# Kernel optimization log

Measured on AMD Instinct MI355X. Metric: run time of the kernel, lower is better.

## Reference

```python
import jax, jax.numpy as jnp
import numpy as np

B, C, H, W = 4, 16, 512, 512
OUT = 16
HID = 64
EPS = 1e-5


def _ln(x, g, b):
    mu = x.mean(-1, keepdims=True)
    v = x.var(-1, keepdims=True)
    return (x - mu) / jnp.sqrt(v + EPS) * g + b


def setup_inputs() -> dict:
    key = jax.random.key(0)
    ks = jax.random.split(key, 8)
    HW = H * W
    d = {}
    d['input'] = jax.random.normal(ks[0], (B, C, H, W), jnp.float32)
    d['W1'] = jax.random.normal(ks[1], (HID, HW), jnp.float32) * 0.01   # Linear1 weight [64, HW]
    d['b1'] = jnp.zeros((HID,), jnp.float32)
    d['ln1_g'] = jnp.ones((HID,), jnp.float32)
    d['ln1_b'] = jnp.zeros((HID,), jnp.float32)
    d['W2'] = jax.random.normal(ks[2], (HW, HID), jnp.float32) * 0.02   # Linear2 weight [HW, 64]
    d['b2'] = jnp.zeros((HW,), jnp.float32)
    d['ln2_g'] = jnp.ones((HW,), jnp.float32)
    d['ln2_b'] = jnp.zeros((HW,), jnp.float32)
    d['cw1'] = jax.random.normal(ks[3], (1, C, 1, 1), jnp.float32) * 0.1   # 1x1 conv C->1
    d['cb1'] = jnp.zeros((1,), jnp.float32)
    d['cw3'] = jax.random.normal(ks[4], (OUT, C, 3, 3), jnp.float32) * 0.05  # 3x3 conv C->OUT
    d['cb3'] = jnp.zeros((OUT,), jnp.float32)
    d['bn_g'] = jnp.ones((OUT,), jnp.float32)
    d['bn_b'] = jnp.zeros((OUT,), jnp.float32)
    return d


def reference(input, W1, b1, ln1_g, ln1_b, W2, b2, ln2_g, ln2_b, cw1, cb1, cw3, cb3, bn_g, bn_b):
    Bq, Cq, Hq, Wq = input.shape
    HW = Hq * Wq
    m = input.reshape(Bq, Cq, HW)
    # Linear1 -> LN -> ReLU  (per-channel over flattened spatial dim)
    h = jax.nn.relu(_ln(m @ W1.T + b1, ln1_g, ln1_b))            # [B, C, 64]
    # Linear2 -> LN -> ReLU
    m2 = jax.nn.relu(_ln(h @ W2.T + b2, ln2_g, ln2_b))           # [B, C, HW]
    m2 = m2.reshape(Bq, Cq, Hq, Wq)
    # 1x1 conv C -> 1
    score = jnp.einsum('bchw,oc->bohw', m2, cw1[:, :, 0, 0]) + cb1[:, None, None]  # [B,1,H,W]
    # keep_topk: ratio 0.25, no grad
    K = HW // 4
    flat = jax.lax.stop_gradient(score.reshape(Bq, HW))
    _, idx = jax.lax.top_k(flat, K)                               # [B, K]
    mask = jnp.zeros_like(flat).at[jnp.arange(Bq)[:, None], idx].set(1.0).reshape(Bq, 1, Hq, Wq)
    # boolean-mask gather: torch selects in ascending flat-index order
    idx_s = jnp.sort(idx, axis=1)                                 # [B, K]
    g = jnp.take_along_axis(m, idx_s[:, None, :], axis=2).reshape(Bq, Cq, Hq // 2, Wq // 2)
    # out_conv: 3x3 conv -> BatchNorm (batch stats, training mode) -> ReLU
    y = jax.lax.conv_general_dilated(g, cw3, (1, 1), [(1, 1), (1, 1)],
                                     dimension_numbers=('NCHW', 'OIHW', 'NCHW'))
    y = y + cb3[:, None, None]
    mu = y.mean((0, 2, 3), keepdims=True)
    v = y.var((0, 2, 3), keepdims=True)
    y = jax.nn.relu((y - mu) / jnp.sqrt(v + EPS) * bn_g[:, None, None] + bn_b[:, None, None])
    return (y, mask)
```

## Files before the change

### kernel.cpp

```cpp
#include <hip/hip_runtime.h>

#define HWN    262144
#define KSEL   65536
#define TIECAP 2048

#define OFF_H      0
#define OFF_DOT1   32768
#define OFF_G      65536
#define OFF_WBAR   98304
#define OFF_WB     98816
#define OFF_SB     99328
#define OFF_MU2    99360
#define OFF_ISIG2  99872
#define OFF_STATE  100384
#define OFF_HIST   100448
#define OFF_TIECNT 116832
#define OFF_CHCNT  116848
#define OFF_TIELST 116864
#define OFF_CHLST  149632
#define OFF_BCNT   182400
#define OFF_BOFF   186496
#define OFF_BNP    190592
#define OFF_BNC    452736
#define OFF_PART2  458752
#define OFF_HT     1015808
#define REGION2    1048576

#define PS_GRAM 4226
#define PS_DOT  4096

typedef double d4_t __attribute__((ext_vector_type(4)));
typedef float  f4v  __attribute__((ext_vector_type(4)));

__device__ __forceinline__ unsigned monokey(double s){
  unsigned long long b = (unsigned long long)__double_as_longlong(s);
  b = (b & 0x8000000000000000ULL) ? ~b : (b | 0x8000000000000000ULL);
  return (unsigned)(b >> 32);
}

__global__ void k_zero(unsigned* hist, unsigned* tiecnt, unsigned* chcnt, unsigned* state){
  int t = threadIdx.x;
  for (int i = t; i < 4096; i += 256) hist[i] = 0u;
  if (t < 4){
    tiecnt[t] = 0u; chcnt[t] = 0u;
    state[t*4+0] = 0u;
    state[t*4+1] = (unsigned)KSEL;
    state[t*4+2] = 0u;
    state[t*4+3] = 0u;
  }
}

__global__ __launch_bounds__(256) void k_mm(const float* __restrict__ W2,
                                            const float* __restrict__ b2,
                                            const float* __restrict__ inp,
                                            const float* __restrict__ W1,
                                            double* __restrict__ partG,
                                            double* __restrict__ partD,
                                            int pPerBlk, int NBH){
  int t = threadIdx.x;
  int w = t >> 6, l = t & 63;
  int q = l >> 4, m = l & 15;
  if ((int)blockIdx.x < NBH){
    int p0 = blockIdx.x * pPerBlk;
    d4_t acc0 = {0.,0.,0.,0.}, acc1 = {0.,0.,0.,0.}, acc2 = {0.,0.,0.,0.};
    d4_t acc3 = {0.,0.,0.,0.}, acc4 = {0.,0.,0.,0.}, acc44 = {0.,0.,0.,0.};
    const float* base = W2 + (size_t)(p0 + q)*64 + m;
    const float* b2p  = b2 + p0 + q;
    int wofs = w*16;
    int nCh = pPerBlk >> 2;
    for (int c = 0; c < nCh; c++){
      double f0 = (double)base[0];
      double f1 = (double)base[16];
      double f2 = (double)base[32];
      double f3 = (double)base[48];
      double fa = (double)base[wofs];
      double bb = (double)b2p[0];
      double f4 = (m == 0) ? bb : ((m == 1) ? 1.0 : 0.0);
      acc0 = __builtin_amdgcn_mfma_f64_16x16x4f64(fa, f0, acc0, 0, 0, 0);
      acc1 = __builtin_amdgcn_mfma_f64_16x16x4f64(fa, f1, acc1, 0, 0, 0);
      acc2 = __builtin_amdgcn_mfma_f64_16x16x4f64(fa, f2, acc2, 0, 0, 0);
      acc3 = __builtin_amdgcn_mfma_f64_16x16x4f64(fa, f3, acc3, 0, 0, 0);
      acc4 = __builtin_amdgcn_mfma_f64_16x16x4f64(fa, f4, acc4, 0, 0, 0);
      if (w == 0)
        acc44 = __builtin_amdgcn_mfma_f64_16x16x4f64(f4, f4, acc44, 0, 0, 0);
      base += 256; b2p += 4;
    }
    d4_t prD = {0.,0.,0.,0.}, pcD = {0.,0.,0.,0.};
    double rp = (double)(1 + m);
    prD = __builtin_amdgcn_mfma_f64_16x16x4f64(rp, 1.0, prD, 0, 0, 0);
    pcD = __builtin_amdgcn_mfma_f64_16x16x4f64(1.0, rp, pcD, 0, 0, 0);
    double* P = partG + (size_t)blockIdx.x * PS_GRAM;
#pragma unroll
    for (int i = 0; i < 4; i++){
      int ri = ((((int)prD[i]) >> 2) - 1) & 15;
      int ci = ((((int)pcD[i]) >> 2) - 1) & 15;
      int r = w*16 + ri;
      P[r*66 +  0 + ci] = acc0[i];
      P[r*66 + 16 + ci] = acc1[i];
      P[r*66 + 32 + ci] = acc2[i];
      P[r*66 + 48 + ci] = acc3[i];
      if (ci < 2) P[r*66 + 64 + ci] = acc4[i];
      if (w == 0 && ri == 0 && ci < 2) P[4224 + ci] = acc44[i];
    }
  } else {
    int blk = (int)blockIdx.x - NBH;
    int p0 = blk * pPerBlk;
    d4_t acc0 = {0.,0.,0.,0.}, acc1 = {0.,0.,0.,0.};
    d4_t acc2 = {0.,0.,0.,0.}, acc3 = {0.,0.,0.,0.};
    const f4v* ap  = (const f4v*)(inp + (size_t)(w*16 + m)*HWN + p0 + q*4);
    const f4v* bp0 = (const f4v*)(W1  + (size_t)( 0 + m)*HWN + p0 + q*4);
    const f4v* bp1 = (const f4v*)(W1  + (size_t)(16 + m)*HWN + p0 + q*4);
    const f4v* bp2 = (const f4v*)(W1  + (size_t)(32 + m)*HWN + p0 + q*4);
    const f4v* bp3 = (const f4v*)(W1  + (size_t)(48 + m)*HWN + p0 + q*4);
    int nCh = pPerBlk >> 4;
    for (int c = 0; c < nCh; c++){
      f4v av = ap [(size_t)c*4];
      f4v b0 = bp0[(size_t)c*4];
      f4v b1 = bp1[(size_t)c*4];
      f4v b2v= bp2[(size_t)c*4];
      f4v b3 = bp3[(size_t)c*4];
#pragma unroll
      for (int t4 = 0; t4 < 4; t4++){
        double a = (double)av[t4];
        acc0 = __builtin_amdgcn_mfma_f64_16x16x4f64(a, (double)b0[t4],  acc0, 0, 0, 0);
        acc1 = __builtin_amdgcn_mfma_f64_16x16x4f64(a, (double)b1[t4],  acc1, 0, 0, 0);
        acc2 = __builtin_amdgcn_mfma_f64_16x16x4f64(a, (double)b2v[t4], acc2, 0, 0, 0);
        acc3 = __builtin_amdgcn_mfma_f64_16x16x4f64(a, (double)b3[t4],  acc3, 0, 0, 0);
      }
    }
    d4_t prD = {0.,0.,0.,0.}, pcD = {0.,0.,0.,0.};
    double rp = (double)(1 + m);
    prD = __builtin_amdgcn_mfma_f64_16x16x4f64(rp, 1.0, prD, 0, 0, 0);
    pcD = __builtin_amdgcn_mfma_f64_16x16x4f64(1.0, rp, pcD, 0, 0, 0);
    double* P = partD + (size_t)blk * PS_DOT;
#pragma unroll
    for (int i = 0; i < 4; i++){
      int ri = ((((int)prD[i]) >> 2) - 1) & 15;
      int ci = ((((int)pcD[i]) >> 2) - 1) & 15;
      int r = w*16 + ri;
      P[r*64 +  0 + ci] = acc0[i];
      P[r*64 + 16 + ci] = acc1[i];
      P[r*64 + 32 + ci] = acc2[i];
      P[r*64 + 48 + ci] = acc3[i];
    }
  }
}

__global__ __launch_bounds__(256) void k_red1(const double* __restrict__ part,
                                              double* __restrict__ part2,
                                              int bPerGrp, int cnt){
  int nj = (cnt + 255) >> 8;
  int jc = blockIdx.x % nj;
  int grp = blockIdx.x / nj;
  int j = jc*256 + threadIdx.x;
  if (j >= cnt) return;
  const double* p = part + (size_t)grp * bPerGrp * cnt + j;
  double s0=0.0, s1=0.0, s2=0.0, s3=0.0;
  for (int b = 0; b < bPerGrp; b += 4){
    s0 += p[(size_t)(b+0)*cnt];
    s1 += p[(size_t)(b+1)*cnt];
    s2 += p[(size_t)(b+2)*cnt];
    s3 += p[(size_t)(b+3)*cnt];
  }
  part2[(size_t)grp*cnt + j] = (s0+s1) + (s2+s3);
}

__global__ void k_redgram2(const double* __restrict__ part2,
                           double* __restrict__ G, double* __restrict__ wb,
                           double* __restrict__ wbar, double* __restrict__ sbv){
  int j = blockIdx.x*256 + threadIdx.x;
  if (j >= PS_GRAM) return;
  double s = 0.0;
#pragma unroll
  for (int b = 0; b < 16; b++) s += part2[(size_t)b*PS_GRAM + j];
  if (j < 4224){
    int r = j / 66, c = j % 66;
    if (c < 64) G[r*64 + c] = s;
    else if (c == 64) wb[r] = s;
    else wbar[r] = s;
  } else if (j == 4224) sbv[1] = s;
  else sbv[0] = s;
}

__global__ void k_reddot2(const double* __restrict__ part2, double* __restrict__ dot1){
  int j = blockIdx.x*256 + threadIdx.x;
  if (j >= PS_DOT) return;
  double s = 0.0;
#pragma unroll
  for (int b = 0; b < 16; b++) s += part2[(size_t)b*PS_DOT + j];
  dot1[j] = s;
}

__global__ void k_h(const double* __restrict__ dot1, const float* __restrict__ b1,
                    const float* __restrict__ g1, const float* __restrict__ b1l,
                    const double* __restrict__ wbar, const double* __restrict__ sbv,
                    double* __restrict__ h, double* __restrict__ hT,
                    double* __restrict__ mu2){
  int r = threadIdx.x;
  double m = 0.0;
  for (int k=0;k<64;k++) m += dot1[r*64+k] + (double)b1[k];
  m *= (1.0/64.0);
  double v = 0.0;
  for (int k=0;k<64;k++){ double d = dot1[r*64+k] + (double)b1[k] - m; v += d*d; }
  v *= (1.0/64.0);
  double inv = 1.0 / sqrt(v + 1e-5);
  double s2 = 0.0;
  for (int k=0;k<64;k++){
    double x = dot1[r*64+k] + (double)b1[k];
    double z = (x - m) * inv;
    double hv = z * (double)g1[k] + (double)b1l[k];
    hv = hv > 0.0 ? hv : 0.0;
    h[r*64+k] = hv;
    hT[k*64+r] = hv;
    s2 += hv * wbar[k];
  }
  mu2[r] = (s2 + sbv[0]) / (double)HWN;
}

__global__ void k_var2(const double* __restrict__ h, const double* __restrict__ G,
                       const double* __restrict__ wb, const double* __restrict__ sbv,
                       const double* __restrict__ mu2, double* __restrict__ isig2){
  int r = blockIdx.x, k = threadIdx.x;
  double hk = h[r*64+k];
  double v = 0.0;
  for (int l=0;l<64;l++) v += G[k*64+l] * h[r*64+l];
  double contrib = hk*v + 2.0*hk*wb[k];
  for (int o=32;o>0;o>>=1) contrib += __shfl_down(contrib, o);
  if (k == 0){
    double E2 = (contrib + sbv[1]) / (double)HWN;
    double mu = mu2[r];
    double var = E2 - mu*mu;
    isig2[r] = 1.0 / sqrt(var + 1e-5);
  }
}

#define SC_K(WF, KIDX) { \
  double w_ = (double)(WF); \
  const double* hp_ = hb + (KIDX)*64; \
  acc[0]+=hp_[0]*w_;  acc[1]+=hp_[1]*w_;  acc[2]+=hp_[2]*w_;  acc[3]+=hp_[3]*w_; \
  acc[4]+=hp_[4]*w_;  acc[5]+=hp_[5]*w_;  acc[6]+=hp_[6]*w_;  acc[7]+=hp_[7]*w_; \
  acc[8]+=hp_[8]*w_;  acc[9]+=hp_[9]*w_;  acc[10]+=hp_[10]*w_; acc[11]+=hp_[11]*w_; \
  acc[12]+=hp_[12]*w_; acc[13]+=hp_[13]*w_; acc[14]+=hp_[14]*w_; acc[15]+=hp_[15]*w_; }

__global__ __launch_bounds__(256) void k_score(const float* __restrict__ W2,
    const float* __restrict__ b2, const float* __restrict__ g2, const float* __restrict__ lb2,
    const float* __restrict__ cw1, const float* __restrict__ cb1,
    const double* __restrict__ hT, const double* __restrict__ mu2, const double* __restrict__ isg,
    double* __restrict__ score, unsigned* __restrict__ key){
  int t = threadIdx.x;
  int p = blockIdx.x*256 + t;
  float4 w4[16];
  const float4* wp = (const float4*)(W2 + (size_t)p*64);
#pragma unroll
  for (int i=0;i<16;i++) w4[i] = wp[i];
  double g2p = (double)g2[p], lb2p = (double)lb2[p], b2p = (double)b2[p];
  double cb = (double)cb1[0];
  for (int b = 0; b < 4; b++){
    double acc[16];
#pragma unroll
    for (int j=0;j<16;j++) acc[j]=0.0;
    const double* hb = hT + b*16;
#pragma unroll
    for (int k4=0;k4<16;k4++){
      float4 wv = w4[k4];
      SC_K(wv.x, (k4*4+0))
      SC_K(wv.y, (k4*4+1))
      SC_K(wv.z, (k4*4+2))
      SC_K(wv.w, (k4*4+3))
    }
    double sc = cb;
#pragma unroll
    for (int j=0;j<16;j++){
      int c = b*16 + j;
      double tv = acc[j] + b2p;
      double z = (tv - mu2[c]) * isg[c];
      double v = z * g2p + lb2p;
      v = v > 0.0 ? v : 0.0;
      sc += v * (double)cw1[j];
    }
    if (sc == 0.0) sc = 0.0;
    score[(size_t)b*HWN + p] = sc;
    key[(size_t)b*HWN + p] = monokey(sc);
  }
}

__global__ void k_hist(const unsigned* __restrict__ key, const unsigned* __restrict__ state,
                       unsigned* __restrict__ hist, int pass){
  __shared__ unsigned lh[256];
  int t = threadIdx.x;
  int b = blockIdx.x >> 7, seg = blockIdx.x & 127;
  lh[t] = 0u;
  __syncthreads();
  unsigned pref = state[b*4+0];
  const unsigned* kb = key + (size_t)b*HWN + seg*2048;
  int shb = 24 - 8*pass;
#pragma unroll
  for (int i=0;i<8;i++){
    unsigned kk = kb[t + 256*i];
    bool ok = (pass == 0) || ((kk >> (32 - 8*pass)) == pref);
    if (ok) atomicAdd(&lh[(kk >> shb) & 255u], 1u);
  }
  __syncthreads();
  atomicAdd(&hist[(pass*4 + b)*256 + t], lh[t]);
}

__global__ void k_scan(unsigned* __restrict__ state, const unsigned* __restrict__ hist, int pass){
  __shared__ unsigned ls[4*256];
  int t = threadIdx.x;
  int b = t >> 8, j = t & 255;
  unsigned cnt = hist[(pass*4 + b)*256 + j];
  int q = 255 - j;
  ls[b*256 + q] = cnt;
  __syncthreads();
  for (int o=1;o<256;o<<=1){
    unsigned v = (q >= o) ? ls[b*256 + q - o] : 0u;
    __syncthreads();
    ls[b*256 + q] += v;
    __syncthreads();
  }
  unsigned need = state[b*4+1];
  unsigned pref = state[b*4+0];
  unsigned GT = (j == 255) ? 0u : ls[b*256 + (254 - j)];
  unsigned GE = ls[b*256 + (255 - j)];
  if (GT < need && need <= GE){
    unsigned npref = (pref << 8) | (unsigned)j;
    state[b*4+0] = npref;
    state[b*4+1] = need - GT;
    if (pass == 3){ state[b*4+2] = npref; state[b*4+3] = need - GT; }
  }
}

__global__ __launch_bounds__(256) void k_mask(const unsigned* __restrict__ key,
    const unsigned* __restrict__ state, float* __restrict__ outM,
    unsigned* __restrict__ bcnt, unsigned* __restrict__ tiecnt, unsigned* __restrict__ tielist){
  __shared__ int red[256];
  int t = threadIdx.x;
  int b = blockIdx.x >> 8, seg = blockIdx.x & 255;
  unsigned T = state[b*4+2];
  int p0 = seg*1024 + t*4;
  size_t base = (size_t)b*HWN + p0;
  uint4 kk = *((const uint4*)(key + base));
  float4 mv; int cnt = 0;
  { int s = kk.x > T; mv.x = s ? 1.f : 0.f; cnt += s;
    if (kk.x == T){ unsigned ti = atomicAdd(&tiecnt[b],1u); if (ti < TIECAP) tielist[b*TIECAP+ti] = (unsigned)(p0+0); } }
  { int s = kk.y > T; mv.y = s ? 1.f : 0.f; cnt += s;
    if (kk.y == T){ unsigned ti = atomicAdd(&tiecnt[b],1u); if (ti < TIECAP) tielist[b*TIECAP+ti] = (unsigned)(p0+1); } }
  { int s = kk.z > T; mv.z = s ? 1.f : 0.f; cnt += s;
    if (kk.z == T){ unsigned ti = atomicAdd(&tiecnt[b],1u); if (ti < TIECAP) tielist[b*TIECAP+ti] = (unsigned)(p0+2); } }
  { int s = kk.w > T; mv.w = s ? 1.f : 0.f; cnt += s;
    if (kk.w == T){ unsigned ti = atomicAdd(&tiecnt[b],1u); if (ti < TIECAP) tielist[b*TIECAP+ti] = (unsigned)(p0+3); } }
  *((float4*)(outM + base)) = mv;
  red[t] = cnt;
  __syncthreads();
  for (int o=128;o>0;o>>=1){ if (t < o) red[t] += red[t+o]; __syncthreads(); }
  if (t == 0) bcnt[b*256 + seg] = (unsigned)red[0];
}

__global__ __launch_bounds__(256) void k_ties(const unsigned* __restrict__ state,
    const unsigned* __restrict__ tiecnt, const unsigned* __restrict__ tielist,
    const double* __restrict__ score, float* __restrict__ outM,
    unsigned* __restrict__ chcnt, unsigned* __restrict__ chlist){
  __shared__ double ssc[TIECAP];
  __shared__ unsigned spp[TIECAP];
  __shared__ unsigned skeep[TIECAP];
  int b = blockIdx.x, t = threadIdx.x;
  unsigned tc = tiecnt[b];
  int n = (int)(tc < (unsigned)TIECAP ? tc : (unsigned)TIECAP);
  unsigned nt = state[b*4+3];
  for (int i=t;i<n;i+=256){
    unsigned p = tielist[b*TIECAP+i];
    spp[i] = p; ssc[i] = score[(size_t)b*HWN + p];
  }
  __syncthreads();
  for (int i=t;i<n;i+=256){
    double si = ssc[i]; unsigned pi = spp[i]; int r = 0;
    for (int j=0;j<n;j++){
      double sj = ssc[j]; unsigned pj = spp[j];
      if (sj > si || (sj == si && pj < pi)) r++;
    }
    skeep[i] = (r < (int)nt) ? 1u : 0u;
  }
  __syncthreads();
  for (int i=t;i<n;i+=256){
    if (skeep[i]){
      unsigned pi = spp[i]; int r2 = 0;
      for (int j=0;j<n;j++) if (skeep[j] && spp[j] < pi) r2++;
      chlist[b*TIECAP + r2] = pi;
      outM[(size_t)b*HWN + pi] = 1.0f;
    }
  }
  if (t == 0){
    unsigned c = ((unsigned)n < nt) ? (unsigned)n : nt;
    chcnt[b] = c;
  }
}

__global__ void k_scanblk(const unsigned* __restrict__ bcnt, unsigned* __restrict__ boff){
  __shared__ unsigned ls[1024];
  int t = threadIdx.x; int b = t >> 8, j = t & 255;
  unsigned own = bcnt[b*256 + j];
  ls[t] = own;
  __syncthreads();
  for (int o=1;o<256;o<<=1){
    unsigned v = (j >= o) ? ls[b*256 + j - o] : 0u;
    __syncthreads();
    ls[t] += v;
    __syncthreads();
  }
  boff[b*256 + j] = ls[t] - own;
}

__device__ __forceinline__ void gath_one(unsigned kv, int p, unsigned T,
    const unsigned* __restrict__ cl, unsigned nch, unsigned base, int& run,
    const float* __restrict__ inp, float* __restrict__ g, int b){
  int isGT = kv > T;
  int isCh = 0;
  if (kv == T && nch > 0u){
    for (unsigned j=0;j<nch;j++) if (cl[j] == (unsigned)p){ isCh = 1; break; }
  }
  if (isGT | isCh){
    unsigned adj = 0;
    for (unsigned j=0;j<nch;j++) adj += (cl[j] < (unsigned)p) ? 1u : 0u;
    unsigned rank = base + (unsigned)run + adj;
#pragma unroll
    for (int c=0;c<16;c++)
      g[(size_t)(b*16+c)*KSEL + rank] = inp[(size_t)(b*16+c)*HWN + p];
  }
  run += isGT;
}

__global__ __launch_bounds__(256) void k_gather(const unsigned* __restrict__ key,
    const unsigned* __restrict__ state, const unsigned* __restrict__ boff,
    const unsigned* __restrict__ chcnt, const unsigned* __restrict__ chlist,
    const float* __restrict__ inp, float* __restrict__ g){
  __shared__ int wt[4];
  int t = threadIdx.x;
  int b = blockIdx.x >> 8, seg = blockIdx.x & 255;
  unsigned T = state[b*4+2];
  int p0 = seg*1024 + t*4;
  uint4 kk = *((const uint4*)(key + (size_t)b*HWN + p0));
  int s0 = kk.x > T, s1 = kk.y > T, s2 = kk.z > T, s3 = kk.w > T;
  int cnt = s0 + s1 + s2 + s3;
  int l = t & 63;
  int incl = cnt;
#pragma unroll
  for (int o=1;o<64;o<<=1){ int v = __shfl_up(incl, o); if (l >= o) incl += v; }
  int w = t >> 6;
  if (l == 63) wt[w] = incl;
  __syncthreads();
  int wex = 0;
#pragma unroll
  for (int i=0;i<4;i++) if (i < w) wex += wt[i];
  int exth = incl - cnt;
  unsigned base = boff[b*256 + seg] + (unsigned)wex + (unsigned)exth;
  unsigned nch = chcnt[b];
  const unsigned* cl = chlist + b*TIECAP;
  int run = 0;
  gath_one(kk.x, p0+0, T, cl, nch, base, run, inp, g, b);
  gath_one(kk.y, p0+1, T, cl, nch, base, run, inp, g, b);
  gath_one(kk.z, p0+2, T, cl, nch, base, run, inp, g, b);
  gath_one(kk.w, p0+3, T, cl, nch, base, run, inp, g, b);
}

__global__ __launch_bounds__(256) void k_conv(const float* __restrict__ g,
    const float* __restrict__ cw3, const float* __restrict__ cb3,
    float* __restrict__ outY, double* __restrict__ bnp){
  __shared__ float wsm[2304];
  __shared__ float it[18*18];
  __shared__ double red[16][4][2];
  int t = threadIdx.x;
  int b = blockIdx.x >> 8, tile = blockIdx.x & 255;
  int ty0 = (tile >> 4) * 16, tx0 = (tile & 15) * 16;
  int tx = t & 15, ty = t >> 4;
#pragma unroll
  for (int i=0;i<9;i++){ int j = t + 256*i; if (j < 2304) wsm[j] = cw3[j]; }
  float acc[16];
#pragma unroll
  for (int i=0;i<16;i++) acc[i] = 0.f;
  for (int ic=0; ic<16; ic++){
    __syncthreads();
    for (int j=t;j<324;j+=256){
      int gy = ty0 - 1 + j/18, gx = tx0 - 1 + (j%18);
      float v = 0.f;
      if (gy >= 0 && gy < 256 && gx >= 0 && gx < 256)
        v = g[(size_t)(b*16+ic)*KSEL + gy*256 + gx];
      it[j] = v;
    }
    __syncthreads();
#pragma unroll
    for (int ky=0;ky<3;ky++)
#pragma unroll
      for (int kx=0;kx<3;kx++){
        float v = it[(ty+ky)*18 + tx+kx];
#pragma unroll
        for (int oc=0;oc<16;oc++) acc[oc] += v * wsm[oc*144 + ic*9 + ky*3 + kx];
      }
  }
  int w = t >> 6, l = t & 63;
  for (int oc=0;oc<16;oc++){
    float yv = acc[oc] + cb3[oc];
    outY[(size_t)(b*16+oc)*KSEL + (ty0+ty)*256 + tx0+tx] = yv;
    double s = (double)yv, q = (double)yv*(double)yv;
    for (int o=32;o>0;o>>=1){ s += __shfl_down(s, o); q += __shfl_down(q, o); }
    if (l == 0){ red[oc][w][0] = s; red[oc][w][1] = q; }
  }
  __syncthreads();
  if (t < 16){
    double s=0.0, q=0.0;
    for (int w2=0;w2<4;w2++){ s += red[t][w2][0]; q += red[t][w2][1]; }
    bnp[(size_t)blockIdx.x*32 + t*2]   = s;
    bnp[(size_t)blockIdx.x*32 + t*2+1] = q;
  }
}

__global__ void k_bnred(const double* __restrict__ bnp, const float* __restrict__ bng,
                        const float* __restrict__ bnb, float* __restrict__ bnc){
  __shared__ double red[16][16][2];
  int t = threadIdx.x; int oc = t >> 4, sl = t & 15;
  double s = 0.0, q = 0.0;
  for (int i=0;i<64;i++){
    int blk = sl*64 + i;
    s += bnp[(size_t)blk*32 + oc*2];
    q += bnp[(size_t)blk*32 + oc*2+1];
  }
  red[oc][sl][0] = s; red[oc][sl][1] = q;
  __syncthreads();
  if (t < 16){
    double S=0.0, Q=0.0;
    for (int i=0;i<16;i++){ S += red[t][i][0]; Q += red[t][i][1]; }
    double N = 262144.0;
    double mu = S/N, var = Q/N - mu*mu;
    double inv = 1.0 / sqrt(var + 1e-5);
    double a = (double)bng[t] * inv;
    double bsh = (double)bnb[t] - mu*a;
    bnc[t*2] = (float)a; bnc[t*2+1] = (float)bsh;
  }
}

__global__ void k_bnapply(float* __restrict__ outY, const float* __restrict__ bnc){
  int i = blockIdx.x*256 + threadIdx.x;
  float4 v = ((float4*)outY)[i];
  int oc = (i >> 14) & 15;
  float a = bnc[oc*2], bsh = bnc[oc*2+1];
  v.x = fmaxf(v.x*a + bsh, 0.f);
  v.y = fmaxf(v.y*a + bsh, 0.f);
  v.z = fmaxf(v.z*a + bsh, 0.f);
  v.w = fmaxf(v.w*a + bsh, 0.f);
  ((float4*)outY)[i] = v;
}

extern "C" void kernel_launch(void* const* d_in, const int* in_sizes, int n_in,
                              void* d_out, int out_size, void* d_ws, size_t ws_size,
                              hipStream_t stream){
  const float* inp  = (const float*)d_in[0];
  const float* W1   = (const float*)d_in[1];
  const float* b1   = (const float*)d_in[2];
  const float* g1   = (const float*)d_in[3];
  const float* b1l  = (const float*)d_in[4];
  const float* W2   = (const float*)d_in[5];
  const float* b2   = (const float*)d_in[6];
  const float* g2   = (const float*)d_in[7];
  const float* lb2  = (const float*)d_in[8];
  const float* cw1  = (const float*)d_in[9];
  const float* cb1  = (const float*)d_in[10];
  const float* cw3  = (const float*)d_in[11];
  const float* cb3  = (const float*)d_in[12];
  const float* bng  = (const float*)d_in[13];
  const float* bnb  = (const float*)d_in[14];
  (void)in_sizes; (void)n_in; (void)out_size;

  char* ws = (char*)d_ws;
  float* outY = (float*)d_out;
  float* outM = outY + 4194304;

  size_t need2048 = (size_t)REGION2 + 2048ull*(PS_GRAM + PS_DOT)*8;
  size_t need512  = (size_t)REGION2 + 512ull*4352*8 + 16777216ull;
  int NBH = (ws_size >= need2048) ? 2048 : ((ws_size >= need512) ? 512 : 128);
  int pPerBlk = HWN / NBH;
  int bPerGrp = NBH / 16;

  double*  partG  = (double*)(ws + REGION2);
  double*  partD  = (double*)(ws + REGION2 + (size_t)NBH*PS_GRAM*8);
  double*  score  = (double*)(ws + REGION2);
  unsigned* key   = (unsigned*)(ws + REGION2 + 8388608ull);
  float*   gbuf   = (float*)(ws + REGION2 + 12582912ull);
  double*  hbuf   = (double*)(ws + OFF_H);
  double*  hTbuf  = (double*)(ws + OFF_HT);
  double*  dot1   = (double*)(ws + OFF_DOT1);
  double*  G      = (double*)(ws + OFF_G);
  double*  wbar   = (double*)(ws + OFF_WBAR);
  double*  wb     = (double*)(ws + OFF_WB);
  double*  sbv    = (double*)(ws + OFF_SB);
  double*  mu2    = (double*)(ws + OFF_MU2);
  double*  isg    = (double*)(ws + OFF_ISIG2);
  unsigned* state = (unsigned*)(ws + OFF_STATE);
  unsigned* hist  = (unsigned*)(ws + OFF_HIST);
  unsigned* tiecnt= (unsigned*)(ws + OFF_TIECNT);
  unsigned* chcnt = (unsigned*)(ws + OFF_CHCNT);
  unsigned* tielist=(unsigned*)(ws + OFF_TIELST);
  unsigned* chlist= (unsigned*)(ws + OFF_CHLST);
  unsigned* bcnt  = (unsigned*)(ws + OFF_BCNT);
  unsigned* boff  = (unsigned*)(ws + OFF_BOFF);
  double*  bnp    = (double*)(ws + OFF_BNP);
  float*   bnc    = (float*)(ws + OFF_BNC);
  double*  part2  = (double*)(ws + OFF_PART2);

  k_zero<<<1, 256, 0, stream>>>(hist, tiecnt, chcnt, state);
  k_mm<<<2*NBH, 256, 0, stream>>>(W2, b2, inp, W1, partG, partD, pPerBlk, NBH);
  k_red1<<<17*16, 256, 0, stream>>>(partG, part2, bPerGrp, PS_GRAM);
  k_redgram2<<<17, 256, 0, stream>>>(part2, G, wb, wbar, sbv);
  k_red1<<<16*16, 256, 0, stream>>>(partD, part2, bPerGrp, PS_DOT);
  k_reddot2<<<16, 256, 0, stream>>>(part2, dot1);
  k_h<<<1, 64, 0, stream>>>(dot1, b1, g1, b1l, wbar, sbv, hbuf, hTbuf, mu2);
  k_var2<<<64, 64, 0, stream>>>(hbuf, G, wb, sbv, mu2, isg);
  k_score<<<1024, 256, 0, stream>>>(W2, b2, g2, lb2, cw1, cb1, hTbuf, mu2, isg, score, key);
  for (int pass = 0; pass < 4; pass++){
    k_hist<<<512, 256, 0, stream>>>(key, state, hist, pass);
    k_scan<<<1, 1024, 0, stream>>>(state, hist, pass);
  }
  k_mask<<<1024, 256, 0, stream>>>(key, state, outM, bcnt, tiecnt, tielist);
  k_ties<<<4, 256, 0, stream>>>(state, tiecnt, tielist, score, outM, chcnt, chlist);
  k_scanblk<<<1, 1024, 0, stream>>>(bcnt, boff);
  k_gather<<<1024, 256, 0, stream>>>(key, state, boff, chcnt, chlist, inp, gbuf);
  k_conv<<<1024, 256, 0, stream>>>(gbuf, cw3, cb3, outY, bnp);
  k_bnred<<<1, 256, 0, stream>>>(bnp, bng, bnb, bnc);
  k_bnapply<<<4096, 256, 0, stream>>>(outY, bnc);
}
```

Before: 450.0 us.

## Software-prefetch next chunk in k_mm loops and cap grid at 512 blocks

Both branches of the fused Gram/dot MFMA kernel now load the next iteration's W2/b2 or input/W1 values into registers before issuing the current iteration's f64 MFMAs, with a peeled final iteration, so global load latency overlaps with matrix math. The host also drops the 2048-block configuration, so each block handles a larger slice of the spatial dimension and fewer partial sums need to be written and reduced. The trade-off is higher register pressure and less parallelism per launch.

```diff
diff --git a/kernel.cpp b/kernel.cpp
--- a/kernel.cpp
+++ b/kernel.cpp
@@ -68,14 +68,15 @@
     const float* b2p  = b2 + p0 + q;
     int wofs = w*16;
     int nCh = pPerBlk >> 2;
-    for (int c = 0; c < nCh; c++){
-      double f0 = (double)base[0];
-      double f1 = (double)base[16];
-      double f2 = (double)base[32];
-      double f3 = (double)base[48];
-      double fa = (double)base[wofs];
-      double bb = (double)b2p[0];
-      double f4 = (m == 0) ? bb : ((m == 1) ? 1.0 : 0.0);
+    float g0 = base[0], g1 = base[16], g2 = base[32], g3 = base[48];
+    float ga = base[wofs], gb = b2p[0];
+    for (int c = 0; c < nCh-1; c++){
+      base += 256; b2p += 4;
+      float n0 = base[0], n1 = base[16], n2 = base[32], n3 = base[48];
+      float na = base[wofs], nb = b2p[0];
+      double f0 = (double)g0, f1 = (double)g1, f2 = (double)g2, f3 = (double)g3;
+      double fa = (double)ga;
+      double f4 = (m == 0) ? (double)gb : ((m == 1) ? 1.0 : 0.0);
       acc0 = __builtin_amdgcn_mfma_f64_16x16x4f64(fa, f0, acc0, 0, 0, 0);
       acc1 = __builtin_amdgcn_mfma_f64_16x16x4f64(fa, f1, acc1, 0, 0, 0);
       acc2 = __builtin_amdgcn_mfma_f64_16x16x4f64(fa, f2, acc2, 0, 0, 0);
@@ -83,7 +84,19 @@
       acc4 = __builtin_amdgcn_mfma_f64_16x16x4f64(fa, f4, acc4, 0, 0, 0);
       if (w == 0)
         acc44 = __builtin_amdgcn_mfma_f64_16x16x4f64(f4, f4, acc44, 0, 0, 0);
-      base += 256; b2p += 4;
+      g0 = n0; g1 = n1; g2 = n2; g3 = n3; ga = na; gb = nb;
+    }
+    {
+      double f0 = (double)g0, f1 = (double)g1, f2 = (double)g2, f3 = (double)g3;
+      double fa = (double)ga;
+      double f4 = (m == 0) ? (double)gb : ((m == 1) ? 1.0 : 0.0);
+      acc0 = __builtin_amdgcn_mfma_f64_16x16x4f64(fa, f0, acc0, 0, 0, 0);
+      acc1 = __builtin_amdgcn_mfma_f64_16x16x4f64(fa, f1, acc1, 0, 0, 0);
+      acc2 = __builtin_amdgcn_mfma_f64_16x16x4f64(fa, f2, acc2, 0, 0, 0);
+      acc3 = __builtin_amdgcn_mfma_f64_16x16x4f64(fa, f3, acc3, 0, 0, 0);
+      acc4 = __builtin_amdgcn_mfma_f64_16x16x4f64(fa, f4, acc4, 0, 0, 0);
+      if (w == 0)
+        acc44 = __builtin_amdgcn_mfma_f64_16x16x4f64(f4, f4, acc44, 0, 0, 0);
     }
     d4_t prD = {0.,0.,0.,0.}, pcD = {0.,0.,0.,0.};
     double rp = (double)(1 + m);
@@ -113,12 +126,10 @@
     const f4v* bp2 = (const f4v*)(W1  + (size_t)(32 + m)*HWN + p0 + q*4);
     const f4v* bp3 = (const f4v*)(W1  + (size_t)(48 + m)*HWN + p0 + q*4);
     int nCh = pPerBlk >> 4;
-    for (int c = 0; c < nCh; c++){
-      f4v av = ap [(size_t)c*4];
-      f4v b0 = bp0[(size_t)c*4];
-      f4v b1 = bp1[(size_t)c*4];
-      f4v b2v= bp2[(size_t)c*4];
-      f4v b3 = bp3[(size_t)c*4];
+    f4v av = ap[0], b0 = bp0[0], b1 = bp1[0], b2v = bp2[0], b3 = bp3[0];
+    for (int c = 0; c < nCh-1; c++){
+      size_t nx = (size_t)(c+1)*4;
+      f4v avn = ap[nx], b0n = bp0[nx], b1n = bp1[nx], b2n = bp2[nx], b3n = bp3[nx];
 #pragma unroll
       for (int t4 = 0; t4 < 4; t4++){
         double a = (double)av[t4];
@@ -127,6 +138,15 @@
         acc2 = __builtin_amdgcn_mfma_f64_16x16x4f64(a, (double)b2v[t4], acc2, 0, 0, 0);
         acc3 = __builtin_amdgcn_mfma_f64_16x16x4f64(a, (double)b3[t4],  acc3, 0, 0, 0);
       }
+      av = avn; b0 = b0n; b1 = b1n; b2v = b2n; b3 = b3n;
+    }
+#pragma unroll
+    for (int t4 = 0; t4 < 4; t4++){
+      double a = (double)av[t4];
+      acc0 = __builtin_amdgcn_mfma_f64_16x16x4f64(a, (double)b0[t4],  acc0, 0, 0, 0);
+      acc1 = __builtin_amdgcn_mfma_f64_16x16x4f64(a, (double)b1[t4],  acc1, 0, 0, 0);
+      acc2 = __builtin_amdgcn_mfma_f64_16x16x4f64(a, (double)b2v[t4], acc2, 0, 0, 0);
+      acc3 = __builtin_amdgcn_mfma_f64_16x16x4f64(a, (double)b3[t4],  acc3, 0, 0, 0);
     }
     d4_t prD = {0.,0.,0.,0.}, pcD = {0.,0.,0.,0.};
     double rp = (double)(1 + m);
@@ -573,9 +593,8 @@
   float* outY = (float*)d_out;
   float* outM = outY + 4194304;
 
-  size_t need2048 = (size_t)REGION2 + 2048ull*(PS_GRAM + PS_DOT)*8;
   size_t need512  = (size_t)REGION2 + 512ull*4352*8 + 16777216ull;
-  int NBH = (ws_size >= need2048) ? 2048 : ((ws_size >= need512) ? 512 : 128);
+  int NBH = (ws_size >= need512) ? 512 : 128;
   int pPerBlk = HWN / NBH;
   int bPerGrp = NBH / 16;
 
```

Measured after the change: 391.8 us. 12.9% less time.
